# Performance work log

Measured on AMD Instinct MI355X. Metric: run time of the kernel, lower is better.

## Reference

```python
import jax, jax.numpy as jnp
import numpy as np

B, T, C = 16, 2048, 68
HEAD = 64

def setup_inputs() -> dict:
    key = jax.random.key(0)
    k1, k2, k3, k4 = jax.random.split(key, 4)
    x = jax.random.normal(k1, (B, T, C), dtype=jnp.float32)
    # Linear(n_embd, head_size, bias=False): y = x @ W, W stored as [C, HEAD]
    Wk = jax.random.normal(k2, (C, HEAD), dtype=jnp.float32) / np.sqrt(C)
    Wq = jax.random.normal(k3, (C, HEAD), dtype=jnp.float32) / np.sqrt(C)
    Wv = jax.random.normal(k4, (C, HEAD), dtype=jnp.float32) / np.sqrt(C)
    return {"x": x, "Wk": Wk, "Wq": Wq, "Wv": Wv}

def reference(x, Wk, Wq, Wv):
    # single-head attention, no causal mask, dropout p=0.0 (identity)
    k = jnp.einsum('btc,ch->bth', x, Wk)   # [B,T,H]
    q = jnp.einsum('btc,ch->bth', x, Wq)   # [B,T,H]
    v = jnp.einsum('btc,ch->bth', x, Wv)   # [B,T,H]
    scale = 1.0 / jnp.sqrt(jnp.asarray(k.shape[-1], k.dtype))
    wei = jnp.einsum('bqh,bkh->bqk', q, k) * scale  # [B,T,T]
    wei = jax.nn.softmax(wei, axis=-1)
    out = jnp.einsum('bqk,bkh->bqh', wei, v)        # [B,T,H]
    return out
```

## Files before the change

### kernel.cpp

```cpp
#include <hip/hip_runtime.h>
#include <hip/hip_bf16.h>

#define BB 16
#define TT 2048
#define CC 68
#define HH 64
#define PP 40

typedef short short8 __attribute__((ext_vector_type(8)));
typedef float floatx4 __attribute__((ext_vector_type(4)));

static __device__ __forceinline__ unsigned short f2bf(float f) {
    union { float f; unsigned u; } v; v.f = f;
    unsigned r = v.u + 0x7fffu + ((v.u >> 16) & 1u);
    return (unsigned short)(r >> 16);
}
static __device__ __forceinline__ unsigned pk2(float a, float b) {
    unsigned ua = __builtin_bit_cast(unsigned, a) + 0x8000u;
    unsigned ub = __builtin_bit_cast(unsigned, b) + 0x8000u;
    return (ua >> 16) | (ub & 0xffff0000u);
}

#define GLD16(gsrc, ldsbase)                                                        \
    __builtin_amdgcn_global_load_lds(                                               \
        (const __attribute__((address_space(1))) unsigned int*)(gsrc),              \
        (__attribute__((address_space(3))) unsigned int*)(ldsbase), 16, 0, 0)

__global__ __launch_bounds__(256) void prep_w(
        const float* __restrict__ Wk, const float* __restrict__ Wq,
        const float* __restrict__ Wv, unsigned short* __restrict__ Wt) {
    int idx = blockIdx.x * 256 + threadIdx.x;
    if (idx >= 192 * 96) return;
    int n = idx / 96, c = idx - n * 96;
    float v = 0.f;
    if (c < CC) {
        if (n < 64)       v = Wk[c * 64 + n];
        else if (n < 128) v = Wq[c * 64 + (n - 64)] * 0.18033688011112042f;
        else              v = Wv[c * 64 + (n - 128)];
    }
    Wt[idx] = f2bf(v);
}

__global__ __launch_bounds__(256) void qkv_kernel(
        const float* __restrict__ x, const unsigned short* __restrict__ Wt,
        unsigned short* __restrict__ Qb, unsigned short* __restrict__ Kb,
        unsigned short* __restrict__ Vt) {
    __shared__ unsigned short xs[64 * 104];
    __shared__ unsigned short wl[192 * 104];

    int tid = threadIdx.x;
    int wave = tid >> 6, lane = tid & 63, quad = lane >> 4, l15 = lane & 15;
    size_t row0 = (size_t)blockIdx.x * 64;
    int b = (int)(row0 >> 11), t0 = (int)(row0 & 2047);

    for (int i = tid; i < 64 * CC; i += 256) {
        int r = i / CC, c = i - r * CC;
        xs[r * 104 + c] = f2bf(x[row0 * CC + i]);
    }
    for (int i = tid; i < 64 * 28; i += 256) {
        int r = i / 28, c = 68 + (i - r * 28);
        xs[r * 104 + c] = 0;
    }
    for (int i = 0; i < 9; ++i) {
        int ci = i * 256 + tid;
        int r = ci / 12, c = ci - r * 12;
        *(short8*)&wl[r * 104 + c * 8] = *(const short8*)&Wt[r * 96 + c * 8];
    }
    __syncthreads();

    short8 a[3];
    #pragma unroll
    for (int cs = 0; cs < 3; ++cs)
        a[cs] = *(const short8*)&xs[(wave * 16 + l15) * 104 + cs * 32 + quad * 8];

    for (int nt = 0; nt < 12; ++nt) {
        floatx4 acc = (floatx4){0.f, 0.f, 0.f, 0.f};
        #pragma unroll
        for (int cs = 0; cs < 3; ++cs) {
            short8 bf = *(const short8*)&wl[(nt * 16 + l15) * 104 + cs * 32 + quad * 8];
            acc = __builtin_amdgcn_mfma_f32_16x16x32_bf16(a[cs], bf, acc, 0, 0, 0);
        }
        if (nt < 8) {
            unsigned short* dst = (nt < 4) ? Kb : Qb;
            int h = (nt & 3) * 16 + l15;
            #pragma unroll
            for (int r = 0; r < 4; ++r)
                dst[(row0 + wave * 16 + quad * 4 + r) * 64 + h] = f2bf(acc[r]);
        } else {
            int h = (nt - 8) * 16 + l15;
            int t = t0 + wave * 16 + quad * 4;
            uint2 v2; v2.x = pk2(acc[0], acc[1]); v2.y = pk2(acc[2], acc[3]);
            *(uint2*)&Vt[((size_t)(b * 64 + h)) * TT + t] = v2;
        }
    }
}

__global__ __launch_bounds__(256) void attn_kernel(
        const unsigned short* __restrict__ Qb,
        const unsigned short* __restrict__ Kb,
        const unsigned short* __restrict__ Vt,
        float* __restrict__ out) {
    __shared__ union {
        struct { unsigned char K[4][4096]; unsigned char V[4][4096]; } s;
        struct { float accL[64][66]; } f;
    } u;
    __shared__ unsigned short Ps[4][32 * PP];
    __shared__ float lL[2][64];

    int tid = threadIdx.x;
    int wave = tid >> 6, lane = tid & 63, quad = lane >> 4, l15 = lane & 15;
    int half = wave >> 1, qh = wave & 1;
    int b = blockIdx.x >> 5, qblk = blockIdx.x & 31;
    int q0 = qblk * 64 + qh * 32;
    int kbase = half * 1024;

    short8 qf[2][2];
    #pragma unroll
    for (int qs = 0; qs < 2; ++qs)
        #pragma unroll
        for (int kh = 0; kh < 2; ++kh)
            qf[qs][kh] = *(const short8*)&Qb[((size_t)(b * TT + q0 + qs * 16 + l15)) * 64
                                             + kh * 32 + quad * 8];

    floatx4 acc[2][4];
    float lpart[2] = {0.f, 0.f};
    #pragma unroll
    for (int qs = 0; qs < 2; ++qs)
        #pragma unroll
        for (int hb = 0; hb < 4; ++hb) acc[qs][hb] = (floatx4){0.f, 0.f, 0.f, 0.f};

    auto stage = [&](int it) {
        int kt = kbase + it * 32;
        int p = it & 1;
        if (qh == 0) {
            unsigned char* base = u.s.K[half * 2 + p];
            #pragma unroll
            for (int i = 0; i < 4; ++i) {
                int ci = i * 64 + lane;
                int kv = ci >> 3, cp = ci & 7, c = cp ^ (kv & 7);
                GLD16(Kb + ((size_t)(b * TT + kt + kv) * 64 + c * 8), base + i * 1024);
            }
        } else {
            unsigned char* base = u.s.V[half * 2 + p];
            #pragma unroll
            for (int i = 0; i < 4; ++i) {
                int ci = i * 64 + lane;
                int h = ci >> 2, cp = ci & 3, c = cp ^ ((h >> 1) & 3);
                GLD16(Vt + ((size_t)(b * 64 + h) * TT + kt + c * 8), base + i * 1024);
            }
        }
    };

    stage(0);
    for (int it = 0; it < 32; ++it) {
        __syncthreads();
        int p = it & 1;
        if (it + 1 < 32) stage(it + 1);

        const unsigned char* KT = u.s.K[half * 2 + p];
        const unsigned char* VT = u.s.V[half * 2 + p];

        short8 kf[2][2];
        #pragma unroll
        for (int ks = 0; ks < 2; ++ks)
            #pragma unroll
            for (int kh = 0; kh < 2; ++kh) {
                int kv = ks * 16 + l15;
                int cp = (kh * 4 + quad) ^ (l15 & 7);
                kf[ks][kh] = *(const short8*)(KT + kv * 128 + cp * 16);
            }

        floatx4 s[2][2];
        #pragma unroll
        for (int qs = 0; qs < 2; ++qs)
            #pragma unroll
            for (int ks = 0; ks < 2; ++ks) {
                floatx4 z = (floatx4){0.f, 0.f, 0.f, 0.f};
                z = __builtin_amdgcn_mfma_f32_16x16x32_bf16(kf[ks][0], qf[qs][0], z, 0, 0, 0);
                z = __builtin_amdgcn_mfma_f32_16x16x32_bf16(kf[ks][1], qf[qs][1], z, 0, 0, 0);
                s[qs][ks] = z;
            }

        #pragma unroll
        for (int qs = 0; qs < 2; ++qs) {
            float lp = 0.f;
            #pragma unroll
            for (int ks = 0; ks < 2; ++ks) {
                float e0 = __builtin_amdgcn_exp2f(s[qs][ks][0]);
                float e1 = __builtin_amdgcn_exp2f(s[qs][ks][1]);
                float e2 = __builtin_amdgcn_exp2f(s[qs][ks][2]);
                float e3 = __builtin_amdgcn_exp2f(s[qs][ks][3]);
                lp += (e0 + e1) + (e2 + e3);
                uint2 w; w.x = pk2(e0, e1); w.y = pk2(e2, e3);
                *(uint2*)&Ps[wave][(qs * 16 + l15) * PP + ks * 16 + quad * 4] = w;
            }
            lpart[qs] += lp;
        }

        short8 vf[4];
        #pragma unroll
        for (int hb = 0; hb < 4; ++hb) {
            int h = hb * 16 + l15;
            int cp = quad ^ ((l15 >> 1) & 3);
            vf[hb] = *(const short8*)(VT + h * 64 + cp * 16);
        }
        #pragma unroll
        for (int qs = 0; qs < 2; ++qs) {
            short8 pf = *(const short8*)&Ps[wave][(qs * 16 + l15) * PP + quad * 8];
            #pragma unroll
            for (int hb = 0; hb < 4; ++hb)
                acc[qs][hb] = __builtin_amdgcn_mfma_f32_16x16x32_bf16(pf, vf[hb], acc[qs][hb], 0, 0, 0);
        }
    }

    #pragma unroll
    for (int qs = 0; qs < 2; ++qs) {
        float v = lpart[qs];
        v += __shfl_xor(v, 16);
        v += __shfl_xor(v, 32);
        lpart[qs] = v;
    }
    if (quad == 0) {
        lL[half][qh * 32 + l15]      = lpart[0];
        lL[half][qh * 32 + 16 + l15] = lpart[1];
    }
    __syncthreads();

    if (half == 1) {
        #pragma unroll
        for (int qs = 0; qs < 2; ++qs)
            #pragma unroll
            for (int hb = 0; hb < 4; ++hb)
                #pragma unroll
                for (int r = 0; r < 4; ++r)
                    u.f.accL[qh * 32 + qs * 16 + quad * 4 + r][hb * 16 + l15] = acc[qs][hb][r];
    }
    __syncthreads();

    if (half == 0) {
        #pragma unroll
        for (int qs = 0; qs < 2; ++qs) {
            float rl[4];
            #pragma unroll
            for (int r = 0; r < 4; ++r) {
                int qw = qh * 32 + qs * 16 + quad * 4 + r;
                rl[r] = 1.0f / (lL[0][qw] + lL[1][qw]);
            }
            #pragma unroll
            for (int hb = 0; hb < 4; ++hb)
                #pragma unroll
                for (int r = 0; r < 4; ++r) {
                    int qw = qh * 32 + qs * 16 + quad * 4 + r;
                    float tot = acc[qs][hb][r] + u.f.accL[qw][hb * 16 + l15];
                    out[((size_t)(b * TT + qblk * 64 + qw)) * 64 + hb * 16 + l15] = tot * rl[r];
                }
        }
    }
}

extern "C" void kernel_launch(void* const* d_in, const int* in_sizes, int n_in,
                              void* d_out, int out_size, void* d_ws, size_t ws_size,
                              hipStream_t stream) {
    const float* x  = (const float*)d_in[0];
    const float* Wk = (const float*)d_in[1];
    const float* Wq = (const float*)d_in[2];
    const float* Wv = (const float*)d_in[3];

    unsigned short* Qb = (unsigned short*)d_ws;
    unsigned short* Kb = Qb + (size_t)BB * TT * HH;
    unsigned short* Vt = Kb + (size_t)BB * TT * HH;
    unsigned short* Wt = Vt + (size_t)BB * TT * HH;
    float* out = (float*)d_out;

    prep_w<<<dim3(72), dim3(256), 0, stream>>>(Wk, Wq, Wv, Wt);
    qkv_kernel<<<dim3(BB * TT / 64), dim3(256), 0, stream>>>(x, Wt, Qb, Kb, Vt);
    attn_kernel<<<dim3(BB * (TT / 64)), dim3(256), 0, stream>>>(Qb, Kb, Vt, out);
}
```

Before: 108.9 us.

## Load K/V fragments straight from global into double-buffered registers, skip LDS staging

The attention kernel no longer stages K and V tiles into LDS with async global-to-LDS copies and a per-iteration block barrier. Each wave now reads its K and V MFMA fragments directly from global memory into registers, prefetching the next tile while computing the current one. Waves that share K/V rows now fetch them separately and depend on cache hits, and register pressure rises. The block index is also remapped to interleave batches, and the QKV projection loads x as float4 and writes packed bf16 pairs.

```diff
diff --git a/kernel.cpp b/kernel.cpp
--- a/kernel.cpp
+++ b/kernel.cpp
@@ -20,11 +20,6 @@
     unsigned ub = __builtin_bit_cast(unsigned, b) + 0x8000u;
     return (ua >> 16) | (ub & 0xffff0000u);
 }
-
-#define GLD16(gsrc, ldsbase)                                                        \
-    __builtin_amdgcn_global_load_lds(                                               \
-        (const __attribute__((address_space(1))) unsigned int*)(gsrc),              \
-        (__attribute__((address_space(3))) unsigned int*)(ldsbase), 16, 0, 0)
 
 __global__ __launch_bounds__(256) void prep_w(
         const float* __restrict__ Wk, const float* __restrict__ Wq,
@@ -53,9 +48,14 @@
     size_t row0 = (size_t)blockIdx.x * 64;
     int b = (int)(row0 >> 11), t0 = (int)(row0 & 2047);
 
-    for (int i = tid; i < 64 * CC; i += 256) {
-        int r = i / CC, c = i - r * CC;
-        xs[r * 104 + c] = f2bf(x[row0 * CC + i]);
+    const float4* xsrc4 = (const float4*)(x + row0 * CC);
+    for (int i = tid; i < 1088; i += 256) {
+        float4 xv = xsrc4[i];
+        int r = i / 17, c4 = i - r * 17;
+        uint2 w;
+        w.x = (unsigned)f2bf(xv.x) | ((unsigned)f2bf(xv.y) << 16);
+        w.y = (unsigned)f2bf(xv.z) | ((unsigned)f2bf(xv.w) << 16);
+        *(uint2*)&xs[r * 104 + c4 * 4] = w;
     }
     for (int i = tid; i < 64 * 28; i += 256) {
         int r = i / 28, c = 68 + (i - r * 28);
@@ -100,19 +100,16 @@
         const unsigned short* __restrict__ Kb,
         const unsigned short* __restrict__ Vt,
         float* __restrict__ out) {
-    __shared__ union {
-        struct { unsigned char K[4][4096]; unsigned char V[4][4096]; } s;
-        struct { float accL[64][66]; } f;
-    } u;
-    __shared__ unsigned short Ps[4][32 * PP];
+    __shared__ union { unsigned short Ps[4][32 * PP]; float accL[64][66]; } u;
     __shared__ float lL[2][64];
 
     int tid = threadIdx.x;
     int wave = tid >> 6, lane = tid & 63, quad = lane >> 4, l15 = lane & 15;
     int half = wave >> 1, qh = wave & 1;
-    int b = blockIdx.x >> 5, qblk = blockIdx.x & 31;
+    int id = blockIdx.x;
+    int b = id & 15, qblk = id >> 4;
     int q0 = qblk * 64 + qh * 32;
-    int kbase = half * 1024;
+    unsigned short* ps = u.Ps[wave];
 
     short8 qf[2][2];
     #pragma unroll
@@ -122,6 +119,21 @@
             qf[qs][kh] = *(const short8*)&Qb[((size_t)(b * TT + q0 + qs * 16 + l15)) * 64
                                              + kh * 32 + quad * 8];
 
+    const unsigned short* kp[2][2];
+    const unsigned short* vp[4];
+    {
+        size_t kOff = ((size_t)(b * TT + half * 1024)) * 64;
+        #pragma unroll
+        for (int ks = 0; ks < 2; ++ks)
+            #pragma unroll
+            for (int kh = 0; kh < 2; ++kh)
+                kp[ks][kh] = Kb + kOff + (ks * 16 + l15) * 64 + kh * 32 + quad * 8;
+        size_t vOff = (size_t)b * 64 * TT + half * 1024;
+        #pragma unroll
+        for (int hb = 0; hb < 4; ++hb)
+            vp[hb] = Vt + vOff + (size_t)(hb * 16 + l15) * TT + quad * 8;
+    }
+
     floatx4 acc[2][4];
     float lpart[2] = {0.f, 0.f};
     #pragma unroll
@@ -129,46 +141,20 @@
         #pragma unroll
         for (int hb = 0; hb < 4; ++hb) acc[qs][hb] = (floatx4){0.f, 0.f, 0.f, 0.f};
 
-    auto stage = [&](int it) {
-        int kt = kbase + it * 32;
-        int p = it & 1;
-        if (qh == 0) {
-            unsigned char* base = u.s.K[half * 2 + p];
-            #pragma unroll
-            for (int i = 0; i < 4; ++i) {
-                int ci = i * 64 + lane;
-                int kv = ci >> 3, cp = ci & 7, c = cp ^ (kv & 7);
-                GLD16(Kb + ((size_t)(b * TT + kt + kv) * 64 + c * 8), base + i * 1024);
-            }
-        } else {
-            unsigned char* base = u.s.V[half * 2 + p];
-            #pragma unroll
-            for (int i = 0; i < 4; ++i) {
-                int ci = i * 64 + lane;
-                int h = ci >> 2, cp = ci & 3, c = cp ^ ((h >> 1) & 3);
-                GLD16(Vt + ((size_t)(b * 64 + h) * TT + kt + c * 8), base + i * 1024);
-            }
-        }
+    auto loadKV = [&](short8 (&kf)[2][2], short8 (&vf)[4], int it) {
+        #pragma unroll
+        for (int ks = 0; ks < 2; ++ks)
+            #pragma unroll
+            for (int kh = 0; kh < 2; ++kh)
+                kf[ks][kh] = *(const short8*)(kp[ks][kh] + it * 2048);
+        #pragma unroll
+        for (int hb = 0; hb < 4; ++hb)
+            vf[hb] = *(const short8*)(vp[hb] + it * 32);
     };
 
-    stage(0);
-    for (int it = 0; it < 32; ++it) {
-        __syncthreads();
-        int p = it & 1;
-        if (it + 1 < 32) stage(it + 1);
-
-        const unsigned char* KT = u.s.K[half * 2 + p];
-        const unsigned char* VT = u.s.V[half * 2 + p];
-
-        short8 kf[2][2];
-        #pragma unroll
-        for (int ks = 0; ks < 2; ++ks)
-            #pragma unroll
-            for (int kh = 0; kh < 2; ++kh) {
-                int kv = ks * 16 + l15;
-                int cp = (kh * 4 + quad) ^ (l15 & 7);
-                kf[ks][kh] = *(const short8*)(KT + kv * 128 + cp * 16);
-            }
+    auto step = [&](short8 (&kf)[2][2], short8 (&vf)[4],
+                    short8 (&kfn)[2][2], short8 (&vfn)[4], int itn) {
+        loadKV(kfn, vfn, itn);
 
         floatx4 s[2][2];
         #pragma unroll
@@ -192,25 +178,29 @@
                 float e3 = __builtin_amdgcn_exp2f(s[qs][ks][3]);
                 lp += (e0 + e1) + (e2 + e3);
                 uint2 w; w.x = pk2(e0, e1); w.y = pk2(e2, e3);
-                *(uint2*)&Ps[wave][(qs * 16 + l15) * PP + ks * 16 + quad * 4] = w;
+                *(uint2*)&ps[(qs * 16 + l15) * PP + ks * 16 + quad * 4] = w;
             }
             lpart[qs] += lp;
         }
 
-        short8 vf[4];
-        #pragma unroll
-        for (int hb = 0; hb < 4; ++hb) {
-            int h = hb * 16 + l15;
-            int cp = quad ^ ((l15 >> 1) & 3);
-            vf[hb] = *(const short8*)(VT + h * 64 + cp * 16);
-        }
-        #pragma unroll
-        for (int qs = 0; qs < 2; ++qs) {
-            short8 pf = *(const short8*)&Ps[wave][(qs * 16 + l15) * PP + quad * 8];
+        short8 pf[2];
+        #pragma unroll
+        for (int qs = 0; qs < 2; ++qs)
+            pf[qs] = *(const short8*)&ps[(qs * 16 + l15) * PP + quad * 8];
+        #pragma unroll
+        for (int qs = 0; qs < 2; ++qs)
             #pragma unroll
             for (int hb = 0; hb < 4; ++hb)
-                acc[qs][hb] = __builtin_amdgcn_mfma_f32_16x16x32_bf16(pf, vf[hb], acc[qs][hb], 0, 0, 0);
-        }
+                acc[qs][hb] = __builtin_amdgcn_mfma_f32_16x16x32_bf16(pf[qs], vf[hb], acc[qs][hb], 0, 0, 0);
+    };
+
+    short8 kfA[2][2], vfA[4], kfB[2][2], vfB[4];
+    loadKV(kfA, vfA, 0);
+    for (int it2 = 0; it2 < 16; ++it2) {
+        int n1 = 2 * it2 + 1;
+        int n2 = (2 * it2 + 2 < 32) ? 2 * it2 + 2 : 31;
+        step(kfA, vfA, kfB, vfB, n1);
+        step(kfB, vfB, kfA, vfA, n2);
     }
 
     #pragma unroll
@@ -233,7 +223,7 @@
             for (int hb = 0; hb < 4; ++hb)
                 #pragma unroll
                 for (int r = 0; r < 4; ++r)
-                    u.f.accL[qh * 32 + qs * 16 + quad * 4 + r][hb * 16 + l15] = acc[qs][hb][r];
+                    u.accL[qh * 32 + qs * 16 + quad * 4 + r][hb * 16 + l15] = acc[qs][hb][r];
     }
     __syncthreads();
 
@@ -251,7 +241,7 @@
                 #pragma unroll
                 for (int r = 0; r < 4; ++r) {
                     int qw = qh * 32 + qs * 16 + quad * 4 + r;
-                    float tot = acc[qs][hb][r] + u.f.accL[qw][hb * 16 + l15];
+                    float tot = acc[qs][hb][r] + u.accL[qw][hb * 16 + l15];
                     out[((size_t)(b * TT + qblk * 64 + qw)) * 64 + hb * 16 + l15] = tot * rl[r];
                 }
         }
```

After: 137.3 us. 1.26x slower.

## Give each attention wave private K/V staging with vmcnt-paced prefetch; register-load QKV inputs

Applied to the files above, without the earlier changes.

The attention kernel changes so that each wave stages its own K and V tiles into a private double buffer, issuing loads two iterations ahead. It waits with explicit s_waitcnt vmcnt instead of a block-wide __syncthreads every iteration, and it remaps block ids so batch is the fast index. The QKV projection kernel drops its LDS staging and reads x rows directly into registers as packed bf16, with W fragments prefetched from global one tile ahead. The aim is to remove per-iteration barriers and LDS round-trips. In exchange, each pair of waves now loads the same K/V tiles twice and the LDS footprint roughly doubles, which may reduce occupancy.

```diff
diff --git a/kernel.cpp b/kernel.cpp
--- a/kernel.cpp
+++ b/kernel.cpp
@@ -25,6 +25,10 @@
     __builtin_amdgcn_global_load_lds(                                               \
         (const __attribute__((address_space(1))) unsigned int*)(gsrc),              \
         (__attribute__((address_space(3))) unsigned int*)(ldsbase), 16, 0, 0)
+
+#define WAITV8 asm volatile("s_waitcnt vmcnt(8)" ::: "memory")
+#define WAITV0 asm volatile("s_waitcnt vmcnt(0)" ::: "memory")
+#define MEMFENCE asm volatile("" ::: "memory")
 
 __global__ __launch_bounds__(256) void prep_w(
         const float* __restrict__ Wk, const float* __restrict__ Wq,
@@ -45,41 +49,47 @@
         const float* __restrict__ x, const unsigned short* __restrict__ Wt,
         unsigned short* __restrict__ Qb, unsigned short* __restrict__ Kb,
         unsigned short* __restrict__ Vt) {
-    __shared__ unsigned short xs[64 * 104];
-    __shared__ unsigned short wl[192 * 104];
-
     int tid = threadIdx.x;
     int wave = tid >> 6, lane = tid & 63, quad = lane >> 4, l15 = lane & 15;
     size_t row0 = (size_t)blockIdx.x * 64;
     int b = (int)(row0 >> 11), t0 = (int)(row0 & 2047);
-
-    for (int i = tid; i < 64 * CC; i += 256) {
-        int r = i / CC, c = i - r * CC;
-        xs[r * 104 + c] = f2bf(x[row0 * CC + i]);
-    }
-    for (int i = tid; i < 64 * 28; i += 256) {
-        int r = i / 28, c = 68 + (i - r * 28);
-        xs[r * 104 + c] = 0;
-    }
-    for (int i = 0; i < 9; ++i) {
-        int ci = i * 256 + tid;
-        int r = ci / 12, c = ci - r * 12;
-        *(short8*)&wl[r * 104 + c * 8] = *(const short8*)&Wt[r * 96 + c * 8];
-    }
-    __syncthreads();
+    size_t myrow = row0 + wave * 16 + l15;
+    const float* xr = x + myrow * CC;
 
     short8 a[3];
-    #pragma unroll
-    for (int cs = 0; cs < 3; ++cs)
-        a[cs] = *(const short8*)&xs[(wave * 16 + l15) * 104 + cs * 32 + quad * 8];
-
+    union { short8 s8; unsigned u[4]; } t;
+    #pragma unroll
+    for (int cs = 0; cs < 2; ++cs) {
+        float4 f0 = *(const float4*)(xr + cs * 32 + quad * 8);
+        float4 f1 = *(const float4*)(xr + cs * 32 + quad * 8 + 4);
+        t.u[0] = pk2(f0.x, f0.y); t.u[1] = pk2(f0.z, f0.w);
+        t.u[2] = pk2(f1.x, f1.y); t.u[3] = pk2(f1.z, f1.w);
+        a[cs] = t.s8;
+    }
+    {
+        t.u[0] = 0; t.u[1] = 0; t.u[2] = 0; t.u[3] = 0;
+        if (quad == 0) {
+            float4 f = *(const float4*)(xr + 64);
+            t.u[0] = pk2(f.x, f.y); t.u[1] = pk2(f.z, f.w);
+        }
+        a[2] = t.s8;
+    }
+
+    auto loadW = [&](short8 (&w)[3], int nt) {
+        #pragma unroll
+        for (int cs = 0; cs < 3; ++cs)
+            w[cs] = *(const short8*)&Wt[(nt * 16 + l15) * 96 + cs * 32 + quad * 8];
+    };
+
+    short8 wf[2][3];
+    loadW(wf[0], 0);
     for (int nt = 0; nt < 12; ++nt) {
+        if (nt + 1 < 12) loadW(wf[(nt + 1) & 1], nt + 1);
         floatx4 acc = (floatx4){0.f, 0.f, 0.f, 0.f};
         #pragma unroll
-        for (int cs = 0; cs < 3; ++cs) {
-            short8 bf = *(const short8*)&wl[(nt * 16 + l15) * 104 + cs * 32 + quad * 8];
-            acc = __builtin_amdgcn_mfma_f32_16x16x32_bf16(a[cs], bf, acc, 0, 0, 0);
-        }
+        for (int cs = 0; cs < 3; ++cs)
+            acc = __builtin_amdgcn_mfma_f32_16x16x32_bf16(a[cs], wf[nt & 1][cs], acc, 0, 0, 0);
+
         if (nt < 8) {
             unsigned short* dst = (nt < 4) ? Kb : Qb;
             int h = (nt & 3) * 16 + l15;
@@ -88,9 +98,9 @@
                 dst[(row0 + wave * 16 + quad * 4 + r) * 64 + h] = f2bf(acc[r]);
         } else {
             int h = (nt - 8) * 16 + l15;
-            int t = t0 + wave * 16 + quad * 4;
+            int tt = t0 + wave * 16 + quad * 4;
             uint2 v2; v2.x = pk2(acc[0], acc[1]); v2.y = pk2(acc[2], acc[3]);
-            *(uint2*)&Vt[((size_t)(b * 64 + h)) * TT + t] = v2;
+            *(uint2*)&Vt[((size_t)(b * 64 + h)) * TT + tt] = v2;
         }
     }
 }
@@ -101,8 +111,8 @@
         const unsigned short* __restrict__ Vt,
         float* __restrict__ out) {
     __shared__ union {
-        struct { unsigned char K[4][4096]; unsigned char V[4][4096]; } s;
-        struct { float accL[64][66]; } f;
+        unsigned char stg[4][2][8192];
+        float accL[64][66];
     } u;
     __shared__ unsigned short Ps[4][32 * PP];
     __shared__ float lL[2][64];
@@ -110,9 +120,11 @@
     int tid = threadIdx.x;
     int wave = tid >> 6, lane = tid & 63, quad = lane >> 4, l15 = lane & 15;
     int half = wave >> 1, qh = wave & 1;
-    int b = blockIdx.x >> 5, qblk = blockIdx.x & 31;
+    int id = blockIdx.x;
+    int b = id & 15, qblk = id >> 4;
     int q0 = qblk * 64 + qh * 32;
     int kbase = half * 1024;
+    unsigned short* ps = Ps[wave];
 
     short8 qf[2][2];
     #pragma unroll
@@ -129,46 +141,40 @@
         #pragma unroll
         for (int hb = 0; hb < 4; ++hb) acc[qs][hb] = (floatx4){0.f, 0.f, 0.f, 0.f};
 
-    auto stage = [&](int it) {
+    auto stage = [&](int it, int p) {
+        unsigned char* base = u.stg[wave][p];
         int kt = kbase + it * 32;
-        int p = it & 1;
-        if (qh == 0) {
-            unsigned char* base = u.s.K[half * 2 + p];
-            #pragma unroll
-            for (int i = 0; i < 4; ++i) {
-                int ci = i * 64 + lane;
-                int kv = ci >> 3, cp = ci & 7, c = cp ^ (kv & 7);
-                GLD16(Kb + ((size_t)(b * TT + kt + kv) * 64 + c * 8), base + i * 1024);
-            }
-        } else {
-            unsigned char* base = u.s.V[half * 2 + p];
-            #pragma unroll
-            for (int i = 0; i < 4; ++i) {
-                int ci = i * 64 + lane;
-                int h = ci >> 2, cp = ci & 3, c = cp ^ ((h >> 1) & 3);
-                GLD16(Vt + ((size_t)(b * 64 + h) * TT + kt + c * 8), base + i * 1024);
-            }
+        #pragma unroll
+        for (int i = 0; i < 4; ++i) {
+            int ci = i * 64 + lane;
+            int kv = ci >> 3, cp = ci & 7, c = cp ^ (kv & 7);
+            GLD16(Kb + ((size_t)(b * TT + kt + kv) * 64 + c * 8), base + i * 1024);
+        }
+        #pragma unroll
+        for (int i = 0; i < 4; ++i) {
+            int ci = i * 64 + lane;
+            int h = ci >> 2, cp = ci & 3, c = cp ^ ((h >> 1) & 3);
+            GLD16(Vt + ((size_t)(b * 64 + h) * TT + kt + c * 8), base + 4096 + i * 1024);
         }
     };
 
-    stage(0);
-    for (int it = 0; it < 32; ++it) {
-        __syncthreads();
-        int p = it & 1;
-        if (it + 1 < 32) stage(it + 1);
-
-        const unsigned char* KT = u.s.K[half * 2 + p];
-        const unsigned char* VT = u.s.V[half * 2 + p];
-
-        short8 kf[2][2];
+    auto compute = [&](int p) {
+        const unsigned char* Kbuf = u.stg[wave][p];
+        const unsigned char* Vbuf = Kbuf + 4096;
+
+        short8 kf[2][2], vf[4];
         #pragma unroll
         for (int ks = 0; ks < 2; ++ks)
             #pragma unroll
             for (int kh = 0; kh < 2; ++kh) {
-                int kv = ks * 16 + l15;
                 int cp = (kh * 4 + quad) ^ (l15 & 7);
-                kf[ks][kh] = *(const short8*)(KT + kv * 128 + cp * 16);
-            }
+                kf[ks][kh] = *(const short8*)(Kbuf + (ks * 16 + l15) * 128 + cp * 16);
+            }
+        #pragma unroll
+        for (int hb = 0; hb < 4; ++hb) {
+            int cp = quad ^ ((l15 >> 1) & 3);
+            vf[hb] = *(const short8*)(Vbuf + (hb * 16 + l15) * 64 + cp * 16);
+        }
 
         floatx4 s[2][2];
         #pragma unroll
@@ -192,26 +198,31 @@
                 float e3 = __builtin_amdgcn_exp2f(s[qs][ks][3]);
                 lp += (e0 + e1) + (e2 + e3);
                 uint2 w; w.x = pk2(e0, e1); w.y = pk2(e2, e3);
-                *(uint2*)&Ps[wave][(qs * 16 + l15) * PP + ks * 16 + quad * 4] = w;
+                *(uint2*)&ps[(qs * 16 + l15) * PP + ks * 16 + quad * 4] = w;
             }
             lpart[qs] += lp;
         }
 
-        short8 vf[4];
-        #pragma unroll
-        for (int hb = 0; hb < 4; ++hb) {
-            int h = hb * 16 + l15;
-            int cp = quad ^ ((l15 >> 1) & 3);
-            vf[hb] = *(const short8*)(VT + h * 64 + cp * 16);
-        }
-        #pragma unroll
-        for (int qs = 0; qs < 2; ++qs) {
-            short8 pf = *(const short8*)&Ps[wave][(qs * 16 + l15) * PP + quad * 8];
+        short8 pf[2];
+        #pragma unroll
+        for (int qs = 0; qs < 2; ++qs)
+            pf[qs] = *(const short8*)&ps[(qs * 16 + l15) * PP + quad * 8];
+        #pragma unroll
+        for (int qs = 0; qs < 2; ++qs)
             #pragma unroll
             for (int hb = 0; hb < 4; ++hb)
-                acc[qs][hb] = __builtin_amdgcn_mfma_f32_16x16x32_bf16(pf, vf[hb], acc[qs][hb], 0, 0, 0);
-        }
-    }
+                acc[qs][hb] = __builtin_amdgcn_mfma_f32_16x16x32_bf16(pf[qs], vf[hb], acc[qs][hb], 0, 0, 0);
+    };
+
+    stage(0, 0);
+    stage(1, 1);
+    for (int it = 0; it < 31; ++it) {
+        WAITV8;
+        compute(it & 1);
+        if (it + 2 < 32) { MEMFENCE; stage(it + 2, it & 1); }
+    }
+    WAITV0;
+    compute(1);
 
     #pragma unroll
     for (int qs = 0; qs < 2; ++qs) {
@@ -233,7 +244,7 @@
             for (int hb = 0; hb < 4; ++hb)
                 #pragma unroll
                 for (int r = 0; r < 4; ++r)
-                    u.f.accL[qh * 32 + qs * 16 + quad * 4 + r][hb * 16 + l15] = acc[qs][hb][r];
+                    u.accL[qh * 32 + qs * 16 + quad * 4 + r][hb * 16 + l15] = acc[qs][hb][r];
     }
     __syncthreads();
 
@@ -251,7 +262,7 @@
                 #pragma unroll
                 for (int r = 0; r < 4; ++r) {
                     int qw = qh * 32 + qs * 16 + quad * 4 + r;
-                    float tot = acc[qs][hb][r] + u.f.accL[qw][hb * 16 + l15];
+                    float tot = acc[qs][hb][r] + u.accL[qw][hb * 16 + l15];
                     out[((size_t)(b * TT + qblk * 64 + qw)) * 64 + hb * 16 + l15] = tot * rl[r];
                 }
         }
```

After: 110.0 us. Within noise of the previous version (+1.1%).
